# Kernel optimization log

Hardware: AMD Instinct MI355X
Metric: run time of the kernel (lower is better)

## Reference

```python
import jax, jax.numpy as jnp
import numpy as np
from jax import lax

T = 16          # timesteps
EPS = 1e-12     # torch F.normalize eps
DN = ('NCHW', 'OIHW', 'NCHW')

def conv2d(x, w, pad):
    return lax.conv_general_dilated(x, w, (1, 1), [(pad, pad), (pad, pad)],
                                    dimension_numbers=DN)

def setup_inputs() -> dict:
    key = jax.random.key(0)
    ks = jax.random.split(key, 7)
    B, C, H, W, K = 16, 512, 14, 14, 64
    return {
        'input_tensor': jax.random.normal(ks[0], (B * T, C, H, W), jnp.float32),
        'centers': jax.random.normal(ks[1], (K, C), jnp.float32) * 0.05,
        'share_w': jax.random.normal(ks[2], (K, C, 1, 1), jnp.float32) * 0.05,
        'share_b': jax.random.uniform(ks[3], (K,), jnp.float32),
        'U_z': jax.random.normal(ks[4], (K, K, 3, 3), jnp.float32) * 0.05,
        'U_r': jax.random.normal(ks[5], (K, K, 3, 3), jnp.float32) * 0.05,
        'U_h': jax.random.normal(ks[6], (K, K, 3, 3), jnp.float32) * 0.05,
    }

def reference(input_tensor, centers, share_w, share_b, U_z, U_r, U_h):
    NT, C, H, W = input_tensor.shape
    B = NT // T
    K = centers.shape[0]

    # soft-assignment pre-activation: 1x1 conv (SAME) -> [B*T, K, H, W]
    wxb = conv2d(input_tensor, share_w, 0) + share_b[None, :, None, None]
    wxb = wxb.reshape(B, T, K, H, W).transpose(1, 0, 2, 3, 4)  # [T,B,K,H,W]

    def gru_step(h, wxb_t):
        z = jax.nn.sigmoid(wxb_t + conv2d(h, U_z, 1))
        r = jax.nn.sigmoid(wxb_t + conv2d(h, U_r, 1))
        hh = jnp.tanh(wxb_t + conv2d(r * h, U_h, 1))
        h_new = (1.0 - z) * hh + z * h
        return h_new, h_new

    h0 = jnp.zeros((B, K, H, W), input_tensor.dtype)
    _, assign = lax.scan(gru_step, h0, wxb)            # [T,B,K,H,W]
    assign = assign.transpose(1, 0, 2, 3, 4).reshape(B * T, K, H * W)

    a_sum = assign.sum(-1, keepdims=True)              # [BT,K,1]
    a = a_sum * centers[None]                          # [BT,K,C]
    feats = input_tensor.reshape(B * T, C, H * W)
    x = jnp.einsum('nks,ncs->nkc', assign, feats)      # [BT,K,C]

    vlad = (x - a).reshape(B, T, K, C).sum(1)          # [B,K,C]
    vlad = vlad / jnp.maximum(jnp.linalg.norm(vlad, axis=2, keepdims=True), EPS)
    vlad = vlad.reshape(B, K * C)
    vlad = vlad / jnp.maximum(jnp.linalg.norm(vlad, axis=1, keepdims=True), EPS)
    return vlad
```

## Files before the change

### kernel.cpp

```cpp
#include <hip/hip_runtime.h>

#define Bc 16
#define Tc 16
#define Cc 512
#define Kc 64
#define Sc 196
#define KS (Kc*Sc)
#define BKS (Bc*Kc*Sc)
#define TBKS (Tc*BKS)
#define GFIN (16*64*512)
#define PART_N (8*GFIN)

#define GPLANE 288
#define GP_TOT (16 + 64*GPLANE + 16)

__device__ __forceinline__ float sigmoid_f(float x) { return 1.f / (1.f + __expf(-x)); }
__device__ __forceinline__ float tanh_f(float x) { return 1.f - 2.f / (__expf(2.f * x) + 1.f); }

__global__ __launch_bounds__(256) void k_transpose_w(const float* __restrict__ w, float* __restrict__ wt) {
    int idx = blockIdx.x * 256 + threadIdx.x;
    if (idx < Kc * Cc) {
        int k = idx & 63, c = idx >> 6;
        wt[idx] = w[k * Cc + c];
    }
}

__global__ __launch_bounds__(256) void k_conv1x1(const float* __restrict__ x, const float* __restrict__ wt,
                                                 const float* __restrict__ bias, float* __restrict__ wxb) {
    __shared__ float Xs[32][64];
    const int tid = threadIdx.x;
    const int gs0 = blockIdx.x * 64;
    const int kw = __builtin_amdgcn_readfirstlane((tid >> 6) << 4);
    const int lane = tid & 63;
    const int gs_c = gs0 + lane;
    const int n_c = gs_c / Sc, s_c = gs_c - n_c * Sc;
    const float* xcol = x + (size_t)n_c * (Cc * Sc) + s_c;
    const int rgrp = (tid >> 6) * 8;

    float acc[16] = {};
    for (int c0 = 0; c0 < Cc; c0 += 32) {
        __syncthreads();
#pragma unroll
        for (int q = 0; q < 8; ++q)
            Xs[rgrp + q][lane] = xcol[(size_t)(c0 + rgrp + q) * Sc];
        __syncthreads();
#pragma unroll 8
        for (int cc = 0; cc < 32; ++cc) {
            const float xv = Xs[cc][lane];
            const float* wp = wt + (size_t)(c0 + cc) * Kc + kw;
#pragma unroll
            for (int i = 0; i < 16; ++i) acc[i] += wp[i] * xv;
        }
    }
    const int gs = gs0 + lane;
    const int n = gs / Sc, s = gs - (gs / Sc) * Sc;
    const int t = n & 15, b = n >> 4;
    float* op = wxb + (((size_t)t * Bc + b) * Kc + kw) * Sc + s;
#pragma unroll
    for (int i = 0; i < 16; ++i)
        op[(size_t)i * Sc] = acc[i] + bias[kw + i];
}

__global__ __launch_bounds__(256) void k_gru_t0(const float* __restrict__ wxb, float* __restrict__ assign) {
    int i = blockIdx.x * 256 + threadIdx.x;
    float4 v = ((const float4*)wxb)[i];
    float4 o;
    o.x = (1.f - sigmoid_f(v.x)) * tanh_f(v.x);
    o.y = (1.f - sigmoid_f(v.y)) * tanh_f(v.y);
    o.z = (1.f - sigmoid_f(v.z)) * tanh_f(v.z);
    o.w = (1.f - sigmoid_f(v.w)) * tanh_f(v.w);
    ((float4*)assign)[i] = o;
}

__device__ __forceinline__ void pad_init(float* lds, int tid, int nthr) {
    float* P = lds + 16;
    for (int i = tid; i < 64 * 92; i += nthr) {
        int kk = i / 92, pid = i - kk * 92;
        int row, col;
        if (pid < 64) { int rr = pid >> 4; row = (rr < 2) ? rr : rr + 14; col = pid & 15; }
        else { int q = pid - 64; row = 2 + (q >> 1); col = (q & 1) ? 15 : 0; }
        P[kk * GPLANE + row * 16 + col] = 0.f;
    }
    if (tid < 16) { lds[tid] = 0.f; lds[GP_TOT - 16 + tid] = 0.f; }
}

__device__ __forceinline__ void stage_plane(float* P, const float* __restrict__ src, int tid, int nthr) {
    const float4* s4p = (const float4*)src;
    for (int q = tid; q < 3136; q += nthr) {
        float4 v = s4p[q];
        int i = q * 4;
        int kk = i / Sc, s = i - kk * Sc;
        float* pp = P + kk * GPLANE;
        float vv[4] = {v.x, v.y, v.z, v.w};
#pragma unroll
        for (int u = 0; u < 4; ++u) {
            int su = s + u;
            int y = su / 14, xx = su - y * 14;
            pp[(y + 2) * 16 + xx + 1] = vv[u];
        }
    }
}

__global__ __launch_bounds__(1024) void k_gru_gates(const float* __restrict__ assign,
        const float* __restrict__ wxb, const float* __restrict__ Uz, const float* __restrict__ Ur,
        float* __restrict__ zb, float* __restrict__ rh, int t) {
    extern __shared__ float lds[];
    float* P = lds + 16;
    float* red = lds + GP_TOT;
    const int b = blockIdx.x;
    const int k0 = blockIdx.y * 4;
    const int tid = threadIdx.x;
    const float* wxb_t = wxb + (size_t)t * BKS;

    const int wv = __builtin_amdgcn_readfirstlane(tid >> 6);
    const int lane = tid & 63;
    const int yq_e = lane >> 2;
    int kE[2], xbE[2], gE[2]; size_t baseE[2]; bool valE[2]; float preE[2];
#pragma unroll
    for (int m = 0; m < 2; ++m) {
        const int o = wv * 2 + m;
        const int kp_o = o >> 4, v = o & 15;
        gE[m] = v >> 3;
        const int r = (v >> 2) & 1, j = v & 3;
        kE[m] = k0 + kp_o * 2 + r;
        xbE[m] = ((lane & 3) << 2) + j;
        valE[m] = (yq_e >= 1 && yq_e <= 14 && xbE[m] >= 1 && xbE[m] <= 14);
        const int s = (yq_e - 1) * 14 + (xbE[m] - 1);
        baseE[m] = ((size_t)b * Kc + kE[m]) * Sc + (valE[m] ? s : 0);
        preE[m] = valE[m] ? wxb_t[baseE[m]] : 0.f;
    }

    pad_init(lds, tid, 1024);
    stage_plane(P, assign + (size_t)(t - 1) * BKS + (size_t)b * KS, tid, 1024);
    __syncthreads();

    const int kp = wv >> 3, kih = wv & 7;
    const int yp = lane >> 2, xq = (lane & 3) << 2;
    const float* uz0 = Uz + (size_t)(k0 + kp * 2) * 576 + kih * 72;
    const float* ur0 = Ur + (size_t)(k0 + kp * 2) * 576 + kih * 72;
    float az[2][4] = {}, ar[2][4] = {};
    const float* Pw = P + (size_t)(kih * 8) * GPLANE + yp * 16 + xq;
#pragma unroll 2
    for (int ki = 0; ki < 8; ++ki) {
        const float* pk = Pw + ki * GPLANE;
#pragma unroll
        for (int dy = 0; dy < 3; ++dy) {
            const float* row = pk + dy * 16;
            float4 m = *(const float4*)row;
            float e0 = row[-1], e4 = row[4];
#pragma unroll
            for (int r = 0; r < 2; ++r) {
                const float* wz = uz0 + r * 576 + ki * 9 + dy * 3;
                float c0 = wz[0], c1 = wz[1], c2 = wz[2];
                az[r][0] += c0*e0  + c1*m.x + c2*m.y;
                az[r][1] += c0*m.x + c1*m.y + c2*m.z;
                az[r][2] += c0*m.y + c1*m.z + c2*m.w;
                az[r][3] += c0*m.z + c1*m.w + c2*e4;
                const float* wr = ur0 + r * 576 + ki * 9 + dy * 3;
                float d0 = wr[0], d1 = wr[1], d2 = wr[2];
                ar[r][0] += d0*e0  + d1*m.x + d2*m.y;
                ar[r][1] += d0*m.x + d1*m.y + d2*m.z;
                ar[r][2] += d0*m.y + d1*m.z + d2*m.w;
                ar[r][3] += d0*m.z + d1*m.w + d2*e4;
            }
        }
    }
    {
        float* rp = red + (size_t)wv * (16 * 64) + lane;
#pragma unroll
        for (int r = 0; r < 2; ++r)
#pragma unroll
            for (int j = 0; j < 4; ++j) {
                rp[(size_t)(r * 4 + j) * 64] = az[r][j];
                rp[(size_t)(8 + r * 4 + j) * 64] = ar[r][j];
            }
    }
    __syncthreads();
    {
#pragma unroll
        for (int m = 0; m < 2; ++m) {
            const int o = wv * 2 + m;
            const int kp_o = o >> 4, v = o & 15;
            float s0 = 0.f;
#pragma unroll
            for (int w8 = 0; w8 < 8; ++w8)
                s0 += red[(size_t)((kp_o * 8 + w8) * 16 + v) * 64 + lane];
            if (valE[m]) {
                float sv = sigmoid_f(preE[m] + s0);
                if (gE[m] == 0) {
                    zb[baseE[m]] = sv;
                } else {
                    float hv = P[(size_t)kE[m] * GPLANE + (yq_e + 1) * 16 + xbE[m]];
                    rh[baseE[m]] = sv * hv;
                }
            }
        }
    }
}

__global__ __launch_bounds__(1024) void k_gru_out(const float* __restrict__ rhin,
        const float* __restrict__ wxb, const float* __restrict__ Uh, const float* __restrict__ zb,
        float* __restrict__ assign, int t) {
    extern __shared__ float lds[];
    float* P = lds + 16;
    float* red = lds + GP_TOT;
    const int b = blockIdx.x;
    const int k0 = blockIdx.y * 4;
    const int tid = threadIdx.x;
    const float* wxb_t = wxb + (size_t)t * BKS;

    const int wv = __builtin_amdgcn_readfirstlane(tid >> 6);
    const int lane = tid & 63;
    const int yq_e = lane >> 2;
    const int kp_oE = wv >> 3, vE = wv & 7;
    const int rE = vE >> 2, jE = vE & 3;
    const int kE = k0 + kp_oE * 2 + rE;
    const int xbE = ((lane & 3) << 2) + jE;
    const bool valE = (yq_e >= 1 && yq_e <= 14 && xbE >= 1 && xbE <= 14);
    const int sE = (yq_e - 1) * 14 + (xbE - 1);
    const size_t baseE = ((size_t)b * Kc + kE) * Sc + (valE ? sE : 0);
    float preE = 0.f, zvE = 0.f, hpE = 0.f;
    if (valE) {
        preE = wxb_t[baseE];
        zvE = zb[baseE];
        hpE = assign[(size_t)(t - 1) * BKS + baseE];
    }

    pad_init(lds, tid, 1024);
    stage_plane(P, rhin + (size_t)b * KS, tid, 1024);
    __syncthreads();

    const int kp = wv >> 3, kih = wv & 7;
    const int yp = lane >> 2, xq = (lane & 3) << 2;
    const float* uh0 = Uh + (size_t)(k0 + kp * 2) * 576 + kih * 72;
    float ah[2][4] = {};
    const float* Pw = P + (size_t)(kih * 8) * GPLANE + yp * 16 + xq;
#pragma unroll 2
    for (int ki = 0; ki < 8; ++ki) {
        const float* pk = Pw + ki * GPLANE;
#pragma unroll
        for (int dy = 0; dy < 3; ++dy) {
            const float* row = pk + dy * 16;
            float4 m = *(const float4*)row;
            float e0 = row[-1], e4 = row[4];
#pragma unroll
            for (int r = 0; r < 2; ++r) {
                const float* wh = uh0 + r * 576 + ki * 9 + dy * 3;
                float c0 = wh[0], c1 = wh[1], c2 = wh[2];
                ah[r][0] += c0*e0  + c1*m.x + c2*m.y;
                ah[r][1] += c0*m.x + c1*m.y + c2*m.z;
                ah[r][2] += c0*m.y + c1*m.z + c2*m.w;
                ah[r][3] += c0*m.z + c1*m.w + c2*e4;
            }
        }
    }
    {
        float* rp = red + (size_t)wv * (8 * 64) + lane;
#pragma unroll
        for (int r = 0; r < 2; ++r)
#pragma unroll
            for (int j = 0; j < 4; ++j)
                rp[(size_t)(r * 4 + j) * 64] = ah[r][j];
    }
    __syncthreads();
    {
        float s0 = 0.f;
#pragma unroll
        for (int w8 = 0; w8 < 8; ++w8)
            s0 += red[(size_t)((kp_oE * 8 + w8) * 8 + vE) * 64 + lane];
        if (valE) {
            float hh = tanh_f(preE + s0);
            assign[(size_t)t * BKS + baseE] = (1.f - zvE) * hh + zvE * hpE;
        }
    }
}

__global__ __launch_bounds__(256) void k_einsum(const float* __restrict__ x, const float* __restrict__ assign,
                                                float* __restrict__ part) {
    extern __shared__ float lds[];
    float* As = lds;
    float* Xs = lds + 196 * 68;
    const int ch = blockIdx.x, tg = blockIdx.y, b = blockIdx.z;
    const int tid = threadIdx.x;
    const int w = tid >> 6, lane = tid & 63;
    const int kt3 = lane >> 3, ct3 = lane & 7;
    const int kbase = kt3 * 8;
    const int cbase = w * 32 + ct3 * 4;
    float4 acc[8] = {};
    for (int tt = 0; tt < 2; ++tt) {
        const int t = tg * 2 + tt;
        const int n = b * Tc + t;
        __syncthreads();
        {
            const float* ap = assign + ((size_t)t * Bc + b) * KS;
            for (int q = tid; q < 3136; q += 256) {
                int kq = q / Sc, s = q - kq * Sc;
                int k4 = kq * 4;
                float4 v;
                v.x = ap[(size_t)(k4 + 0) * Sc + s];
                v.y = ap[(size_t)(k4 + 1) * Sc + s];
                v.z = ap[(size_t)(k4 + 2) * Sc + s];
                v.w = ap[(size_t)(k4 + 3) * Sc + s];
                *(float4*)(As + (size_t)s * 68 + k4) = v;
            }
        }
        for (int sc = 0; sc < 7; ++sc) {
            const int sb = sc * 28;
            __syncthreads();
            {
                const int c = tid & 127, sh = tid >> 7;
                const float* xp = x + ((size_t)n * Cc + ch * 128 + c) * Sc + sb + sh * 16;
                const int nf = sh ? 3 : 4;
                for (int f = 0; f < nf; ++f) {
                    float4 v = *(const float4*)(xp + f * 4);
                    float* dst = Xs + (size_t)(sh * 16 + f * 4) * 132 + c;
                    dst[0] = v.x; dst[132] = v.y; dst[264] = v.z; dst[396] = v.w;
                }
            }
            __syncthreads();
#pragma unroll 4
            for (int s = 0; s < 28; ++s) {
                const float* ap = As + (size_t)(sb + s) * 68 + kbase;
                float4 a0 = *(const float4*)ap;
                float4 a1 = *(const float4*)(ap + 4);
                float4 xv = *(const float4*)(Xs + (size_t)s * 132 + cbase);
                float av[8] = {a0.x,a0.y,a0.z,a0.w,a1.x,a1.y,a1.z,a1.w};
#pragma unroll
                for (int i = 0; i < 8; ++i) {
                    acc[i].x += av[i] * xv.x;
                    acc[i].y += av[i] * xv.y;
                    acc[i].z += av[i] * xv.z;
                    acc[i].w += av[i] * xv.w;
                }
            }
        }
    }
#pragma unroll
    for (int i = 0; i < 8; ++i) {
        const int k = kbase + i;
        float* op = part + (((size_t)tg * Bc + b) * Kc + k) * Cc + ch * 128 + cbase;
        *(float4*)op = acc[i];
    }
}

__global__ __launch_bounds__(256) void k_reduce(const float* __restrict__ assign, const float* __restrict__ part,
        const float* __restrict__ centers, float* __restrict__ vlad, float* __restrict__ norm2) {
    __shared__ float redw[4];
    __shared__ float a_s;
    const int blk = blockIdx.x;
    const int b = blk >> 6, k = blk & 63;
    const int tid = threadIdx.x;
    const int wave = tid >> 6, lane = tid & 63;
    const size_t bkoff = ((size_t)b * Kc + k) * Sc;
    float s = 0.f;
    for (int q = tid; q < 784; q += 256) {
        int t = q / 49, s4 = q - t * 49;
        float4 v = *(const float4*)(assign + (size_t)t * BKS + bkoff + s4 * 4);
        s += (v.x + v.y) + (v.z + v.w);
    }
#pragma unroll
    for (int o = 1; o < 64; o <<= 1) s += __shfl_xor(s, o);
    if (lane == 0) redw[wave] = s;
    __syncthreads();
    if (tid == 0) a_s = redw[0] + redw[1] + redw[2] + redw[3];
    __syncthreads();
    const float a = a_s;
    const size_t base = ((size_t)b * Kc + k) * Cc;
    const int c = tid * 2;
    float2 acc2 = make_float2(0.f, 0.f);
#pragma unroll
    for (int g = 0; g < 8; ++g) {
        float2 p = *(const float2*)(part + (size_t)g * GFIN + base + c);
        acc2.x += p.x; acc2.y += p.y;
    }
    float2 cv = *(const float2*)(centers + (size_t)k * Cc + c);
    float v0 = acc2.x - a * cv.x, v1 = acc2.y - a * cv.y;
    *(float2*)(vlad + base + c) = make_float2(v0, v1);
    float ss = v0 * v0 + v1 * v1;
#pragma unroll
    for (int o = 1; o < 64; o <<= 1) ss += __shfl_xor(ss, o);
    __syncthreads();
    if (lane == 0) redw[wave] = ss;
    __syncthreads();
    if (tid == 0) norm2[blk] = redw[0] + redw[1] + redw[2] + redw[3];
}

__global__ __launch_bounds__(64) void k_norms(const float* __restrict__ norm2, float* __restrict__ scl) {
    const int b = blockIdx.x;
    const int k = threadIdx.x;
    float ss = norm2[b * Kc + k];
    float inv = 1.f / fmaxf(sqrtf(ss), 1e-12f);
    float g = ss * inv * inv;
#pragma unroll
    for (int o = 1; o < 64; o <<= 1) g += __shfl_xor(g, o);
    float gi = 1.f / fmaxf(sqrtf(g), 1e-12f);
    scl[b * Kc + k] = inv * gi;
}

__global__ __launch_bounds__(256) void k_scale(const float* __restrict__ vlad, const float* __restrict__ scl,
                                               float* __restrict__ out) {
    const int blk = blockIdx.x;
    const int b = blk >> 4, kt = blk & 15;
    const int tid = threadIdx.x;
    const int kk = tid >> 6, lane = tid & 63;
    const int k = kt * 4 + kk;
    const float sv = scl[b * Kc + k];
    const float* vp = vlad + ((size_t)b * Kc + k) * Cc + lane * 8;
    float* op = out + ((size_t)b * Kc + k) * Cc + lane * 8;
    float4 v0 = *(const float4*)vp;
    float4 v1 = *(const float4*)(vp + 4);
    *(float4*)op = make_float4(v0.x * sv, v0.y * sv, v0.z * sv, v0.w * sv);
    *(float4*)(op + 4) = make_float4(v1.x * sv, v1.y * sv, v1.z * sv, v1.w * sv);
}

extern "C" void kernel_launch(void* const* d_in, const int* in_sizes, int n_in,
                              void* d_out, int out_size, void* d_ws, size_t ws_size,
                              hipStream_t stream) {
    (void)in_sizes; (void)n_in; (void)out_size; (void)ws_size;
    const float* x       = (const float*)d_in[0];
    const float* centers = (const float*)d_in[1];
    const float* share_w = (const float*)d_in[2];
    const float* share_b = (const float*)d_in[3];
    const float* Uz      = (const float*)d_in[4];
    const float* Ur      = (const float*)d_in[5];
    const float* Uh      = (const float*)d_in[6];
    float* out = (float*)d_out;
    float* ws  = (float*)d_ws;

    float* part   = ws;
    float* wxb    = ws;
    float* vlad   = ws;
    float* assign = ws + (size_t)PART_N;
    float* zb     = assign + (size_t)TBKS;
    float* rh     = zb + (size_t)BKS;
    float* wt     = rh + (size_t)BKS;
    float* norm2  = wt + (size_t)Kc * Cc;
    float* scl    = norm2 + (size_t)Bc * Kc;

    const size_t gates_lds = (size_t)(GP_TOT + 16 * 16 * 64) * 4;
    const size_t outk_lds  = (size_t)(GP_TOT + 16 * 8 * 64) * 4;
    const size_t ein_lds   = (size_t)(196 * 68 + 28 * 132) * 4;

    k_transpose_w<<<dim3((Kc * Cc + 255) / 256), 256, 0, stream>>>(share_w, wt);
    k_conv1x1<<<dim3(784), 256, 0, stream>>>(x, wt, share_b, wxb);
    k_gru_t0<<<dim3(196), 256, 0, stream>>>(wxb, assign);
    for (int t = 1; t < Tc; ++t) {
        k_gru_gates<<<dim3(16, 16), 1024, gates_lds, stream>>>(assign, wxb, Uz, Ur, zb, rh, t);
        k_gru_out<<<dim3(16, 16), 1024, outk_lds, stream>>>(rh, wxb, Uh, zb, assign, t);
    }
    k_einsum<<<dim3(4, 8, 16), 256, ein_lds, stream>>>(x, assign, part);
    k_reduce<<<dim3(Bc * Kc), 256, 0, stream>>>(assign, part, centers, vlad, norm2);
    k_norms<<<dim3(Bc), 64, 0, stream>>>(norm2, scl);
    k_scale<<<dim3(256), 256, 0, stream>>>(vlad, scl, out);
}
```

Measured before the change: 565.8 us.

## Keep GRU hidden state in pre-padded global planes and halve gate block size

The GRU hidden state and r*h are now stored in global memory already laid out as zero-padded 16x18 planes, so each step kernel copies them into LDS with plain float4 loads. This replaces the per-step padding initialisation and the scatter with divisions. The gate and output kernels drop from 1024 to 512 threads, and each wave now covers 4 output channels instead of 2, with a float4-based cross-wave reduction. The 1x1 conv also prefetches the next 64-channel slab into registers while computing the current one, which adds register pressure and doubles the shared tile.

```diff
diff --git a/kernel.cpp b/kernel.cpp
--- a/kernel.cpp
+++ b/kernel.cpp
@@ -10,9 +10,8 @@
 #define TBKS (Tc*BKS)
 #define GFIN (16*64*512)
 #define PART_N (8*GFIN)
-
-#define GPLANE 288
-#define GP_TOT (16 + 64*GPLANE + 16)
+#define PL 288
+#define PLB (Kc*PL)
 
 __device__ __forceinline__ float sigmoid_f(float x) { return 1.f / (1.f + __expf(-x)); }
 __device__ __forceinline__ float tanh_f(float x) { return 1.f - 2.f / (__expf(2.f * x) + 1.f); }
@@ -27,250 +26,233 @@
 
 __global__ __launch_bounds__(256) void k_conv1x1(const float* __restrict__ x, const float* __restrict__ wt,
                                                  const float* __restrict__ bias, float* __restrict__ wxb) {
-    __shared__ float Xs[32][64];
+    __shared__ float Xs[64][64];
     const int tid = threadIdx.x;
     const int gs0 = blockIdx.x * 64;
     const int kw = __builtin_amdgcn_readfirstlane((tid >> 6) << 4);
     const int lane = tid & 63;
+    const int rbase = (tid >> 6) * 16;
     const int gs_c = gs0 + lane;
     const int n_c = gs_c / Sc, s_c = gs_c - n_c * Sc;
     const float* xcol = x + (size_t)n_c * (Cc * Sc) + s_c;
-    const int rgrp = (tid >> 6) * 8;
-
+
+    float xr[16];
+#pragma unroll
+    for (int q = 0; q < 16; ++q) xr[q] = xcol[(size_t)(rbase + q) * Sc];
     float acc[16] = {};
-    for (int c0 = 0; c0 < Cc; c0 += 32) {
+    for (int c0 = 0; c0 < Cc; c0 += 64) {
         __syncthreads();
 #pragma unroll
-        for (int q = 0; q < 8; ++q)
-            Xs[rgrp + q][lane] = xcol[(size_t)(c0 + rgrp + q) * Sc];
+        for (int q = 0; q < 16; ++q) Xs[rbase + q][lane] = xr[q];
         __syncthreads();
+        if (c0 + 64 < Cc) {
+#pragma unroll
+            for (int q = 0; q < 16; ++q) xr[q] = xcol[(size_t)(c0 + 64 + rbase + q) * Sc];
+        }
 #pragma unroll 8
-        for (int cc = 0; cc < 32; ++cc) {
+        for (int cc = 0; cc < 64; ++cc) {
             const float xv = Xs[cc][lane];
             const float* wp = wt + (size_t)(c0 + cc) * Kc + kw;
 #pragma unroll
             for (int i = 0; i < 16; ++i) acc[i] += wp[i] * xv;
         }
     }
-    const int gs = gs0 + lane;
-    const int n = gs / Sc, s = gs - (gs / Sc) * Sc;
-    const int t = n & 15, b = n >> 4;
-    float* op = wxb + (((size_t)t * Bc + b) * Kc + kw) * Sc + s;
+    const int t = n_c & 15, bb = n_c >> 4;
+    float* op = wxb + (((size_t)t * Bc + bb) * Kc + kw) * Sc + s_c;
 #pragma unroll
     for (int i = 0; i < 16; ++i)
         op[(size_t)i * Sc] = acc[i] + bias[kw + i];
 }
 
-__global__ __launch_bounds__(256) void k_gru_t0(const float* __restrict__ wxb, float* __restrict__ assign) {
-    int i = blockIdx.x * 256 + threadIdx.x;
-    float4 v = ((const float4*)wxb)[i];
-    float4 o;
-    o.x = (1.f - sigmoid_f(v.x)) * tanh_f(v.x);
-    o.y = (1.f - sigmoid_f(v.y)) * tanh_f(v.y);
-    o.z = (1.f - sigmoid_f(v.z)) * tanh_f(v.z);
-    o.w = (1.f - sigmoid_f(v.w)) * tanh_f(v.w);
-    ((float4*)assign)[i] = o;
-}
-
-__device__ __forceinline__ void pad_init(float* lds, int tid, int nthr) {
-    float* P = lds + 16;
-    for (int i = tid; i < 64 * 92; i += nthr) {
-        int kk = i / 92, pid = i - kk * 92;
-        int row, col;
-        if (pid < 64) { int rr = pid >> 4; row = (rr < 2) ? rr : rr + 14; col = pid & 15; }
-        else { int q = pid - 64; row = 2 + (q >> 1); col = (q & 1) ? 15 : 0; }
-        P[kk * GPLANE + row * 16 + col] = 0.f;
-    }
-    if (tid < 16) { lds[tid] = 0.f; lds[GP_TOT - 16 + tid] = 0.f; }
-}
-
-__device__ __forceinline__ void stage_plane(float* P, const float* __restrict__ src, int tid, int nthr) {
-    const float4* s4p = (const float4*)src;
-    for (int q = tid; q < 3136; q += nthr) {
-        float4 v = s4p[q];
-        int i = q * 4;
-        int kk = i / Sc, s = i - kk * Sc;
-        float* pp = P + kk * GPLANE;
-        float vv[4] = {v.x, v.y, v.z, v.w};
-#pragma unroll
-        for (int u = 0; u < 4; ++u) {
-            int su = s + u;
-            int y = su / 14, xx = su - y * 14;
-            pp[(y + 2) * 16 + xx + 1] = vv[u];
-        }
-    }
-}
-
-__global__ __launch_bounds__(1024) void k_gru_gates(const float* __restrict__ assign,
-        const float* __restrict__ wxb, const float* __restrict__ Uz, const float* __restrict__ Ur,
-        float* __restrict__ zb, float* __restrict__ rh, int t) {
+__global__ __launch_bounds__(64) void k_gru_t0(const float* __restrict__ wxb,
+        float* __restrict__ hplane, float* __restrict__ rhplane, float* __restrict__ assign) {
+    const int blk = blockIdx.x;
+    const size_t pbase = (size_t)blk * PL;
+    const size_t cbase = (size_t)blk * Sc;
+    for (int i = threadIdx.x; i < PL; i += 64) {
+        int y = i >> 4, xx = i & 15;
+        float v = 0.f;
+        if (y >= 2 && y <= 15 && xx >= 1 && xx <= 14) {
+            int s = (y - 2) * 14 + (xx - 1);
+            float pre = wxb[cbase + s];
+            v = (1.f - sigmoid_f(pre)) * tanh_f(pre);
+            assign[cbase + s] = v;
+        }
+        hplane[pbase + i] = v;
+        rhplane[pbase + i] = 0.f;
+    }
+}
+
+__global__ __launch_bounds__(512) void k_gru_gates(const float* __restrict__ hplane,
+        const float* __restrict__ wxb_t, const float* __restrict__ Uz, const float* __restrict__ Ur,
+        float* __restrict__ zb, float* __restrict__ rhplane) {
     extern __shared__ float lds[];
-    float* P = lds + 16;
-    float* red = lds + GP_TOT;
+    float* P = lds;
+    float* red = lds + PLB;
     const int b = blockIdx.x;
     const int k0 = blockIdx.y * 4;
     const int tid = threadIdx.x;
-    const float* wxb_t = wxb + (size_t)t * BKS;
-
     const int wv = __builtin_amdgcn_readfirstlane(tid >> 6);
     const int lane = tid & 63;
-    const int yq_e = lane >> 2;
-    int kE[2], xbE[2], gE[2]; size_t baseE[2]; bool valE[2]; float preE[2];
-#pragma unroll
-    for (int m = 0; m < 2; ++m) {
-        const int o = wv * 2 + m;
-        const int kp_o = o >> 4, v = o & 15;
-        gE[m] = v >> 3;
-        const int r = (v >> 2) & 1, j = v & 3;
-        kE[m] = k0 + kp_o * 2 + r;
-        xbE[m] = ((lane & 3) << 2) + j;
-        valE[m] = (yq_e >= 1 && yq_e <= 14 && xbE[m] >= 1 && xbE[m] <= 14);
-        const int s = (yq_e - 1) * 14 + (xbE[m] - 1);
-        baseE[m] = ((size_t)b * Kc + kE[m]) * Sc + (valE[m] ? s : 0);
-        preE[m] = valE[m] ? wxb_t[baseE[m]] : 0.f;
-    }
-
-    pad_init(lds, tid, 1024);
-    stage_plane(P, assign + (size_t)(t - 1) * BKS + (size_t)b * KS, tid, 1024);
-    __syncthreads();
-
-    const int kp = wv >> 3, kih = wv & 7;
+
+    float preE[4]; bool validE[4]; size_t baseE[4]; int pxE[4], setE[4];
+#pragma unroll
+    for (int q = 0; q < 4; ++q) {
+        const int o = tid + q * 512;
+        setE[q] = o >> 8; pxE[q] = o & 255;
+        const int yq = pxE[q] >> 4, xb = pxE[q] & 15;
+        validE[q] = (yq >= 1 && yq <= 14 && xb >= 1 && xb <= 14);
+        const int kk = setE[q] >> 1;
+        const int s = (yq - 1) * 14 + (xb - 1);
+        baseE[q] = ((size_t)b * Kc + k0 + kk) * Sc + (validE[q] ? s : 0);
+        preE[q] = validE[q] ? wxb_t[baseE[q]] : 0.f;
+    }
+    {
+        const float4* src = (const float4*)(hplane + (size_t)b * PLB);
+        float4* dst = (float4*)P;
+        for (int q = tid; q < PLB / 4; q += 512) dst[q] = src[q];
+    }
+    __syncthreads();
+
     const int yp = lane >> 2, xq = (lane & 3) << 2;
-    const float* uz0 = Uz + (size_t)(k0 + kp * 2) * 576 + kih * 72;
-    const float* ur0 = Ur + (size_t)(k0 + kp * 2) * 576 + kih * 72;
-    float az[2][4] = {}, ar[2][4] = {};
-    const float* Pw = P + (size_t)(kih * 8) * GPLANE + yp * 16 + xq;
+    const float* uzb = Uz + (size_t)k0 * 576 + wv * 72;
+    const float* urb = Ur + (size_t)k0 * 576 + wv * 72;
+    float acc[4][2][4] = {};
+    const float* Pw = P + (size_t)(wv * 8) * PL + yp * 16 + xq;
 #pragma unroll 2
-    for (int ki = 0; ki < 8; ++ki) {
-        const float* pk = Pw + ki * GPLANE;
+    for (int ki8 = 0; ki8 < 8; ++ki8) {
+        const float* pk = Pw + ki8 * PL;
 #pragma unroll
         for (int dy = 0; dy < 3; ++dy) {
             const float* row = pk + dy * 16;
             float4 m = *(const float4*)row;
             float e0 = row[-1], e4 = row[4];
 #pragma unroll
-            for (int r = 0; r < 2; ++r) {
-                const float* wz = uz0 + r * 576 + ki * 9 + dy * 3;
+            for (int kk = 0; kk < 4; ++kk) {
+                const float* wz = uzb + kk * 576 + ki8 * 9 + dy * 3;
                 float c0 = wz[0], c1 = wz[1], c2 = wz[2];
-                az[r][0] += c0*e0  + c1*m.x + c2*m.y;
-                az[r][1] += c0*m.x + c1*m.y + c2*m.z;
-                az[r][2] += c0*m.y + c1*m.z + c2*m.w;
-                az[r][3] += c0*m.z + c1*m.w + c2*e4;
-                const float* wr = ur0 + r * 576 + ki * 9 + dy * 3;
+                acc[kk][0][0] += c0*e0  + c1*m.x + c2*m.y;
+                acc[kk][0][1] += c0*m.x + c1*m.y + c2*m.z;
+                acc[kk][0][2] += c0*m.y + c1*m.z + c2*m.w;
+                acc[kk][0][3] += c0*m.z + c1*m.w + c2*e4;
+                const float* wr = urb + kk * 576 + ki8 * 9 + dy * 3;
                 float d0 = wr[0], d1 = wr[1], d2 = wr[2];
-                ar[r][0] += d0*e0  + d1*m.x + d2*m.y;
-                ar[r][1] += d0*m.x + d1*m.y + d2*m.z;
-                ar[r][2] += d0*m.y + d1*m.z + d2*m.w;
-                ar[r][3] += d0*m.z + d1*m.w + d2*e4;
+                acc[kk][1][0] += d0*e0  + d1*m.x + d2*m.y;
+                acc[kk][1][1] += d0*m.x + d1*m.y + d2*m.z;
+                acc[kk][1][2] += d0*m.y + d1*m.z + d2*m.w;
+                acc[kk][1][3] += d0*m.z + d1*m.w + d2*e4;
             }
         }
     }
     {
-        float* rp = red + (size_t)wv * (16 * 64) + lane;
-#pragma unroll
-        for (int r = 0; r < 2; ++r)
-#pragma unroll
-            for (int j = 0; j < 4; ++j) {
-                rp[(size_t)(r * 4 + j) * 64] = az[r][j];
-                rp[(size_t)(8 + r * 4 + j) * 64] = ar[r][j];
-            }
-    }
-    __syncthreads();
-    {
-#pragma unroll
-        for (int m = 0; m < 2; ++m) {
-            const int o = wv * 2 + m;
-            const int kp_o = o >> 4, v = o & 15;
-            float s0 = 0.f;
-#pragma unroll
-            for (int w8 = 0; w8 < 8; ++w8)
-                s0 += red[(size_t)((kp_o * 8 + w8) * 16 + v) * 64 + lane];
-            if (valE[m]) {
-                float sv = sigmoid_f(preE[m] + s0);
-                if (gE[m] == 0) {
-                    zb[baseE[m]] = sv;
-                } else {
-                    float hv = P[(size_t)kE[m] * GPLANE + (yq_e + 1) * 16 + xbE[m]];
-                    rh[baseE[m]] = sv * hv;
-                }
-            }
-        }
-    }
-}
-
-__global__ __launch_bounds__(1024) void k_gru_out(const float* __restrict__ rhin,
-        const float* __restrict__ wxb, const float* __restrict__ Uh, const float* __restrict__ zb,
-        float* __restrict__ assign, int t) {
+        float* rp = red + (size_t)wv * 2048 + lane * 4;
+#pragma unroll
+        for (int kk = 0; kk < 4; ++kk)
+#pragma unroll
+            for (int g = 0; g < 2; ++g)
+                *(float4*)(rp + (kk * 2 + g) * 256) =
+                    make_float4(acc[kk][g][0], acc[kk][g][1], acc[kk][g][2], acc[kk][g][3]);
+    }
+    __syncthreads();
+#pragma unroll
+    for (int q = 0; q < 4; ++q) {
+        const float* rp = red + setE[q] * 256 + pxE[q];
+        float s0 = 0.f;
+#pragma unroll
+        for (int w8 = 0; w8 < 8; ++w8) s0 += rp[(size_t)w8 * 2048];
+        if (validE[q]) {
+            float sv = sigmoid_f(preE[q] + s0);
+            const int kk = setE[q] >> 1;
+            const int k = k0 + kk;
+            if ((setE[q] & 1) == 0) {
+                zb[baseE[q]] = sv;
+            } else {
+                const int yq = pxE[q] >> 4, xb = pxE[q] & 15;
+                float hv = P[(size_t)k * PL + (yq + 1) * 16 + xb];
+                rhplane[(size_t)b * PLB + (size_t)k * PL + (yq + 1) * 16 + xb] = sv * hv;
+            }
+        }
+    }
+}
+
+__global__ __launch_bounds__(512) void k_gru_out(const float* __restrict__ rhplane,
+        const float* __restrict__ wxb_t, const float* __restrict__ Uh, const float* __restrict__ zb,
+        float* __restrict__ hplane, float* __restrict__ assign_t) {
     extern __shared__ float lds[];
-    float* P = lds + 16;
-    float* red = lds + GP_TOT;
+    float* P = lds;
+    float* red = lds + PLB;
     const int b = blockIdx.x;
     const int k0 = blockIdx.y * 4;
     const int tid = threadIdx.x;
-    const float* wxb_t = wxb + (size_t)t * BKS;
-
     const int wv = __builtin_amdgcn_readfirstlane(tid >> 6);
     const int lane = tid & 63;
-    const int yq_e = lane >> 2;
-    const int kp_oE = wv >> 3, vE = wv & 7;
-    const int rE = vE >> 2, jE = vE & 3;
-    const int kE = k0 + kp_oE * 2 + rE;
-    const int xbE = ((lane & 3) << 2) + jE;
-    const bool valE = (yq_e >= 1 && yq_e <= 14 && xbE >= 1 && xbE <= 14);
-    const int sE = (yq_e - 1) * 14 + (xbE - 1);
-    const size_t baseE = ((size_t)b * Kc + kE) * Sc + (valE ? sE : 0);
-    float preE = 0.f, zvE = 0.f, hpE = 0.f;
-    if (valE) {
-        preE = wxb_t[baseE];
-        zvE = zb[baseE];
-        hpE = assign[(size_t)(t - 1) * BKS + baseE];
-    }
-
-    pad_init(lds, tid, 1024);
-    stage_plane(P, rhin + (size_t)b * KS, tid, 1024);
-    __syncthreads();
-
-    const int kp = wv >> 3, kih = wv & 7;
+
+    float preE[2], zvE[2], hpE[2]; bool validE[2]; size_t baseE[2], pposE[2]; int pxE[2], setE[2];
+#pragma unroll
+    for (int q = 0; q < 2; ++q) {
+        const int o = tid + q * 512;
+        setE[q] = o >> 8; pxE[q] = o & 255;
+        const int yq = pxE[q] >> 4, xb = pxE[q] & 15;
+        validE[q] = (yq >= 1 && yq <= 14 && xb >= 1 && xb <= 14);
+        const int s = (yq - 1) * 14 + (xb - 1);
+        const int k = k0 + setE[q];
+        baseE[q] = ((size_t)b * Kc + k) * Sc + (validE[q] ? s : 0);
+        pposE[q] = (size_t)b * PLB + (size_t)k * PL + (yq + 1) * 16 + xb;
+        preE[q] = 0.f; zvE[q] = 0.f; hpE[q] = 0.f;
+        if (validE[q]) {
+            preE[q] = wxb_t[baseE[q]];
+            zvE[q] = zb[baseE[q]];
+            hpE[q] = hplane[pposE[q]];
+        }
+    }
+    {
+        const float4* src = (const float4*)(rhplane + (size_t)b * PLB);
+        float4* dst = (float4*)P;
+        for (int q = tid; q < PLB / 4; q += 512) dst[q] = src[q];
+    }
+    __syncthreads();
+
     const int yp = lane >> 2, xq = (lane & 3) << 2;
-    const float* uh0 = Uh + (size_t)(k0 + kp * 2) * 576 + kih * 72;
-    float ah[2][4] = {};
-    const float* Pw = P + (size_t)(kih * 8) * GPLANE + yp * 16 + xq;
+    const float* uhb = Uh + (size_t)k0 * 576 + wv * 72;
+    float acc[4][4] = {};
+    const float* Pw = P + (size_t)(wv * 8) * PL + yp * 16 + xq;
 #pragma unroll 2
-    for (int ki = 0; ki < 8; ++ki) {
-        const float* pk = Pw + ki * GPLANE;
+    for (int ki8 = 0; ki8 < 8; ++ki8) {
+        const float* pk = Pw + ki8 * PL;
 #pragma unroll
         for (int dy = 0; dy < 3; ++dy) {
             const float* row = pk + dy * 16;
             float4 m = *(const float4*)row;
             float e0 = row[-1], e4 = row[4];
 #pragma unroll
-            for (int r = 0; r < 2; ++r) {
-                const float* wh = uh0 + r * 576 + ki * 9 + dy * 3;
+            for (int kk = 0; kk < 4; ++kk) {
+                const float* wh = uhb + kk * 576 + ki8 * 9 + dy * 3;
                 float c0 = wh[0], c1 = wh[1], c2 = wh[2];
-                ah[r][0] += c0*e0  + c1*m.x + c2*m.y;
-                ah[r][1] += c0*m.x + c1*m.y + c2*m.z;
-                ah[r][2] += c0*m.y + c1*m.z + c2*m.w;
-                ah[r][3] += c0*m.z + c1*m.w + c2*e4;
+                acc[kk][0] += c0*e0  + c1*m.x + c2*m.y;
+                acc[kk][1] += c0*m.x + c1*m.y + c2*m.z;
+                acc[kk][2] += c0*m.y + c1*m.z + c2*m.w;
+                acc[kk][3] += c0*m.z + c1*m.w + c2*e4;
             }
         }
     }
     {
-        float* rp = red + (size_t)wv * (8 * 64) + lane;
-#pragma unroll
-        for (int r = 0; r < 2; ++r)
-#pragma unroll
-            for (int j = 0; j < 4; ++j)
-                rp[(size_t)(r * 4 + j) * 64] = ah[r][j];
-    }
-    __syncthreads();
-    {
+        float* rp = red + (size_t)wv * 1024 + lane * 4;
+#pragma unroll
+        for (int kk = 0; kk < 4; ++kk)
+            *(float4*)(rp + kk * 256) = make_float4(acc[kk][0], acc[kk][1], acc[kk][2], acc[kk][3]);
+    }
+    __syncthreads();
+#pragma unroll
+    for (int q = 0; q < 2; ++q) {
+        const float* rp = red + setE[q] * 256 + pxE[q];
         float s0 = 0.f;
 #pragma unroll
-        for (int w8 = 0; w8 < 8; ++w8)
-            s0 += red[(size_t)((kp_oE * 8 + w8) * 8 + vE) * 64 + lane];
-        if (valE) {
-            float hh = tanh_f(preE + s0);
-            assign[(size_t)t * BKS + baseE] = (1.f - zvE) * hh + zvE * hpE;
+        for (int w8 = 0; w8 < 8; ++w8) s0 += rp[(size_t)w8 * 1024];
+        if (validE[q]) {
+            float hh = tanh_f(preE[q] + s0);
+            float hn = (1.f - zvE[q]) * hh + zvE[q] * hpE[q];
+            hplane[pposE[q]] = hn;
+            assign_t[baseE[q]] = hn;
         }
     }
 }
@@ -427,26 +409,29 @@
     float* out = (float*)d_out;
     float* ws  = (float*)d_ws;
 
-    float* part   = ws;
-    float* wxb    = ws;
-    float* vlad   = ws;
-    float* assign = ws + (size_t)PART_N;
-    float* zb     = assign + (size_t)TBKS;
-    float* rh     = zb + (size_t)BKS;
-    float* wt     = rh + (size_t)BKS;
-    float* norm2  = wt + (size_t)Kc * Cc;
-    float* scl    = norm2 + (size_t)Bc * Kc;
-
-    const size_t gates_lds = (size_t)(GP_TOT + 16 * 16 * 64) * 4;
-    const size_t outk_lds  = (size_t)(GP_TOT + 16 * 8 * 64) * 4;
+    float* part    = ws;
+    float* vlad    = ws;
+    float* wxb     = ws;
+    float* rhplane = ws + (size_t)TBKS;
+    float* assign  = ws + (size_t)PART_N;
+    float* zb      = assign + (size_t)TBKS;
+    float* hplane  = zb + (size_t)BKS;
+    float* wt      = hplane + (size_t)Bc * PLB;
+    float* norm2   = wt + (size_t)Kc * Cc;
+    float* scl     = norm2 + (size_t)Bc * Kc;
+
+    const size_t gates_lds = (size_t)(PLB + 8 * 8 * 256) * 4;
+    const size_t outk_lds  = (size_t)(PLB + 8 * 4 * 256) * 4;
     const size_t ein_lds   = (size_t)(196 * 68 + 28 * 132) * 4;
 
-    k_transpose_w<<<dim3((Kc * Cc + 255) / 256), 256, 0, stream>>>(share_w, wt);
+    k_transpose_w<<<dim3(128), 256, 0, stream>>>(share_w, wt);
     k_conv1x1<<<dim3(784), 256, 0, stream>>>(x, wt, share_b, wxb);
-    k_gru_t0<<<dim3(196), 256, 0, stream>>>(wxb, assign);
+    k_gru_t0<<<dim3(1024), 64, 0, stream>>>(wxb, hplane, rhplane, assign);
     for (int t = 1; t < Tc; ++t) {
-        k_gru_gates<<<dim3(16, 16), 1024, gates_lds, stream>>>(assign, wxb, Uz, Ur, zb, rh, t);
-        k_gru_out<<<dim3(16, 16), 1024, outk_lds, stream>>>(rh, wxb, Uh, zb, assign, t);
+        k_gru_gates<<<dim3(16, 16), 512, gates_lds, stream>>>(hplane, wxb + (size_t)t * BKS,
+                                                              Uz, Ur, zb, rhplane);
+        k_gru_out<<<dim3(16, 16), 512, outk_lds, stream>>>(rhplane, wxb + (size_t)t * BKS,
+                                                           Uh, zb, hplane, assign + (size_t)t * BKS);
     }
     k_einsum<<<dim3(4, 8, 16), 256, ein_lds, stream>>>(x, assign, part);
     k_reduce<<<dim3(Bc * Kc), 256, 0, stream>>>(assign, part, centers, vlad, norm2);
```

New measurement: 530.1 us. 1.07x faster.
